# Performance work log

Hardware: AMD Instinct MI355X
Metric: run time of the kernel (lower is better)

Reference implementation:

```python
import jax, jax.numpy as jnp
import numpy as np

B, T, D = 2, 2048, 1024
N, H = 16, 64  # num_heads, head_dim
LOG2E = 1.442695041
NEG_INF = -1.0e9


def setup_inputs() -> dict:
    key = jax.random.key(0)
    ks = jax.random.split(key, 6)
    return {
        "input_tensor": jax.random.normal(ks[0], (B, T, D), dtype=jnp.float32),
        "attention_mask": jax.random.randint(ks[1], (B, 1, T, T), 0, 2, dtype=jnp.int32),
        "wq": jax.random.normal(ks[2], (D, N, H), dtype=jnp.float32),
        "bq": jnp.zeros((N, H), dtype=jnp.float32),
        "wk": jax.random.normal(ks[3], (D, N, H), dtype=jnp.float32),
        "bk": jnp.zeros((N, H), dtype=jnp.float32),
        "wv": jax.random.normal(ks[4], (D, N, H), dtype=jnp.float32),
        "bv": jnp.zeros((N, H), dtype=jnp.float32),
        "wo": jax.random.normal(ks[5], (D, N, H), dtype=jnp.float32),
        "bo": jnp.zeros((D,), dtype=jnp.float32),
        "per_dim_scale": jnp.zeros((H,), dtype=jnp.float32),
    }


def reference(input_tensor, attention_mask, wq, bq, wk, bk, wv, bv, wo, bo, per_dim_scale):
    # QKV projections: [B,T,D] x [D,N,H] -> [B,T,N,H]
    q = jnp.einsum('btd,dnh->btnh', input_tensor, wq) + bq
    k = jnp.einsum('btd,dnh->btnh', input_tensor, wk) + bk
    v = jnp.einsum('btd,dnh->btnh', input_tensor, wv) + bv
    # per-dim query scaling: (log2(e)/sqrt(H)) * softplus(per_dim_scale)
    scale = (LOG2E / jnp.sqrt(jnp.asarray(H, q.dtype))) * jax.nn.softplus(per_dim_scale)
    q = q * scale
    # scores: [B,N,T,S]
    scores = jnp.einsum('btnh,bsnh->bnts', q, k)
    scores = jnp.where(attention_mask == 0, jnp.asarray(NEG_INF, scores.dtype), scores)
    weights = jax.nn.softmax(scores, axis=-1)
    # AV: [B,N,T,S] x [B,S,N,H] -> [B,T,N,H]
    attn_out = jnp.einsum('bnts,bsnh->btnh', weights, v)
    # output projection: [B,T,N,H] x [D,N,H] -> [B,T,D]
    return jnp.einsum('btnh,dnh->btd', attn_out, wo) + bo
```

## Files before the change

### kernel.cpp

```cpp
#include <hip/hip_runtime.h>
#include <math.h>

typedef __bf16 bf16;
typedef __attribute__((ext_vector_type(8))) __bf16 bf16x8;
typedef __attribute__((ext_vector_type(4))) __bf16 bf16x4;
typedef __attribute__((ext_vector_type(4))) float f32x4;

#define BB 2
#define TT 2048
#define DD 1024
#define NHD 16
#define HD 64
#define MM (BB*TT)
#define LOG2E_F 1.442695041f
#define NEGINF_F (-1.0e9f)

__device__ __forceinline__ void gld16(const bf16* g, bf16* l)
{
    __builtin_amdgcn_global_load_lds(
        (const __attribute__((address_space(1))) unsigned int*)g,
        (__attribute__((address_space(3))) unsigned int*)l, 16, 0, 0);
}

__global__ __launch_bounds__(256)
void prep_all(const float* __restrict__ X, const int* __restrict__ m,
              const float* __restrict__ wq, const float* __restrict__ wk,
              const float* __restrict__ wv, const float* __restrict__ wo,
              bf16* __restrict__ Xh, bf16* __restrict__ Xl,
              bf16* __restrict__ qkh, bf16* __restrict__ qkl,
              bf16* __restrict__ vh, bf16* __restrict__ ob,
              bf16* __restrict__ madd)
{
    __shared__ float tile[32][33];
    const int bid = blockIdx.x;
    const int t   = threadIdx.x;

    if (bid < 4096) {
        int i = bid * 256 + t;
        float4 v = ((const float4*)X)[i];
        float f[4] = {v.x, v.y, v.z, v.w};
        bf16x4 h, l;
        #pragma unroll
        for (int j = 0; j < 4; ++j) {
            bf16 hh = (bf16)f[j];
            h[j] = hh;
            l[j] = (bf16)(f[j] - (float)hh);
        }
        *(bf16x4*)(Xh + (size_t)i * 4) = h;
        *(bf16x4*)(Xl + (size_t)i * 4) = l;
        return;
    }
    if (bid < 8192) {
        const int idx = bid - 4096;
        const int z   = idx >> 10;
        const int bx  = (idx & 31) << 5;
        const int by  = ((idx >> 5) & 31) << 5;
        const int r   = t >> 3;
        const int c4  = (t & 7) << 2;
        if (z == 3) {
            float4 v = *(const float4*)(wo + (size_t)(by + r) * 1024 + bx + c4);
            bf16x4 o = { (bf16)v.x, (bf16)v.y, (bf16)v.z, (bf16)v.w };
            *(bf16x4*)(ob + (size_t)(by + r) * 1024 + bx + c4) = o;
            return;
        }
        const float* src = (z == 0) ? wq : ((z == 1) ? wk : wv);
        bf16* oh = (z == 0) ? qkh : ((z == 1) ? qkh + 1048576 : vh);
        bf16* ol = (z == 0) ? qkl : ((z == 1) ? qkl + 1048576 : nullptr);
        float4 v = *(const float4*)(src + (size_t)(by + r) * 1024 + bx + c4);
        tile[r][c4+0] = v.x; tile[r][c4+1] = v.y;
        tile[r][c4+2] = v.z; tile[r][c4+3] = v.w;
        __syncthreads();
        bf16x4 hv, lv;
        #pragma unroll
        for (int j = 0; j < 4; ++j) {
            float f = tile[c4 + j][r];
            bf16 h = (bf16)f;
            hv[j] = h;
            lv[j] = (bf16)(f - (float)h);
        }
        *(bf16x4*)(oh + (size_t)(bx + r) * 1024 + by + c4) = hv;
        if (ol)
            *(bf16x4*)(ol + (size_t)(bx + r) * 1024 + by + c4) = lv;
        return;
    }
    {
        int i = (bid - 8192) * 256 + t;
        const int4* mp = (const int4*)m + (size_t)i * 2;
        int4 a  = mp[0];
        int4 b4 = mp[1];
        bf16x8 o;
        o[0] = (bf16)(a.x  ? 0.f : NEGINF_F);
        o[1] = (bf16)(a.y  ? 0.f : NEGINF_F);
        o[2] = (bf16)(a.z  ? 0.f : NEGINF_F);
        o[3] = (bf16)(a.w  ? 0.f : NEGINF_F);
        o[4] = (bf16)(b4.x ? 0.f : NEGINF_F);
        o[5] = (bf16)(b4.y ? 0.f : NEGINF_F);
        o[6] = (bf16)(b4.z ? 0.f : NEGINF_F);
        o[7] = (bf16)(b4.w ? 0.f : NEGINF_F);
        *(bf16x8*)(madd + (size_t)i * 8) = o;
    }
}

__global__ __launch_bounds__(256)
void gemm_proj(const bf16* __restrict__ Xh, const bf16* __restrict__ Xl,
               const bf16* __restrict__ Wh, const bf16* __restrict__ Wl,
               const bf16* __restrict__ Wvh,
               const float* __restrict__ bq, const float* __restrict__ bk,
               const float* __restrict__ bv, const float* __restrict__ pds,
               bf16* __restrict__ oQh, bf16* __restrict__ oQl,
               bf16* __restrict__ oKh, bf16* __restrict__ oKl,
               bf16* __restrict__ oVt)
{
    __shared__ bf16 S[4][128 * 32];

    const int bid  = blockIdx.x;
    const int t    = threadIdx.x;
    const int lane = t & 63;
    const int w    = t >> 6;
    const int quad = lane >> 4, l15 = lane & 15;
    const int wm   = (w >> 1) << 6;
    const int wn   = (w & 1)  << 6;

    const int jr0 = ((w * 2 + 0) << 4) + (lane >> 2);
    const int jr1 = ((w * 2 + 1) << 4) + (lane >> 2);
    const int kch = (lane & 3) << 3;
    const int off0 = (w * 2 + 0) * 512;
    const int off1 = (w * 2 + 1) * 512;

    if (bid < 512) {
        const int m0 = (bid >> 4) << 7;
        const int n0 = (bid & 15) << 7;
        bf16* Ah = S[0]; bf16* Al = S[1]; bf16* Bh = S[2]; bf16* Bl = S[3];

        const bf16* pAh0 = Xh + (size_t)(m0 + jr0) * DD + kch;
        const bf16* pAh1 = Xh + (size_t)(m0 + jr1) * DD + kch;
        const bf16* pAl0 = Xl + (size_t)(m0 + jr0) * DD + kch;
        const bf16* pAl1 = Xl + (size_t)(m0 + jr1) * DD + kch;
        const bf16* pBh0 = Wh + (size_t)(n0 + jr0) * DD + kch;
        const bf16* pBh1 = Wh + (size_t)(n0 + jr1) * DD + kch;
        const bf16* pBl0 = Wl + (size_t)(n0 + jr0) * DD + kch;
        const bf16* pBl1 = Wl + (size_t)(n0 + jr1) * DD + kch;

        f32x4 acc[4][4] = {};

        for (int k0 = 0; k0 < DD; k0 += 32) {
            __syncthreads();
            gld16(pAh0 + k0, Ah + off0);  gld16(pAh1 + k0, Ah + off1);
            gld16(pAl0 + k0, Al + off0);  gld16(pAl1 + k0, Al + off1);
            gld16(pBh0 + k0, Bh + off0);  gld16(pBh1 + k0, Bh + off1);
            gld16(pBl0 + k0, Bl + off0);  gld16(pBl1 + k0, Bl + off1);
            __syncthreads();

            bf16x8 ah[4], bh[4];
            #pragma unroll
            for (int mt = 0; mt < 4; ++mt)
                ah[mt] = *(const bf16x8*)(Ah + (wm + (mt << 4) + l15) * 32 + (quad << 3));
            #pragma unroll
            for (int nt = 0; nt < 4; ++nt)
                bh[nt] = *(const bf16x8*)(Bh + (wn + (nt << 4) + l15) * 32 + (quad << 3));
            #pragma unroll
            for (int mt = 0; mt < 4; ++mt)
                #pragma unroll
                for (int nt = 0; nt < 4; ++nt)
                    acc[mt][nt] = __builtin_amdgcn_mfma_f32_16x16x32_bf16(
                        ah[mt], bh[nt], acc[mt][nt], 0, 0, 0);

            bf16x8 bl[4];
            #pragma unroll
            for (int nt = 0; nt < 4; ++nt)
                bl[nt] = *(const bf16x8*)(Bl + (wn + (nt << 4) + l15) * 32 + (quad << 3));
            #pragma unroll
            for (int mt = 0; mt < 4; ++mt)
                #pragma unroll
                for (int nt = 0; nt < 4; ++nt)
                    acc[mt][nt] = __builtin_amdgcn_mfma_f32_16x16x32_bf16(
                        ah[mt], bl[nt], acc[mt][nt], 0, 0, 0);

            bf16x8 al[4];
            #pragma unroll
            for (int mt = 0; mt < 4; ++mt)
                al[mt] = *(const bf16x8*)(Al + (wm + (mt << 4) + l15) * 32 + (quad << 3));
            #pragma unroll
            for (int mt = 0; mt < 4; ++mt)
                #pragma unroll
                for (int nt = 0; nt < 4; ++nt)
                    acc[mt][nt] = __builtin_amdgcn_mfma_f32_16x16x32_bf16(
                        al[mt], bh[nt], acc[mt][nt], 0, 0, 0);
        }

        #pragma unroll
        for (int nt = 0; nt < 4; ++nt) {
            const int col = n0 + wn + (nt << 4) + l15;
            const int isQ = (col < 1024);
            const int nh  = col & 1023;
            const int n   = nh >> 6, h = nh & 63;
            const float bcol = isQ ? bq[nh] : bk[nh];
            float s = 1.f;
            if (isQ) {
                float x  = pds[h];
                float sp = fmaxf(x, 0.f) + log1pf(expf(-fabsf(x)));
                s = (LOG2E_F * LOG2E_F / 8.0f) * sp;
            }
            bf16* dH = isQ ? oQh : oKh;
            bf16* dL = isQ ? oQl : oKl;
            #pragma unroll
            for (int mt = 0; mt < 4; ++mt) {
                #pragma unroll
                for (int reg = 0; reg < 4; ++reg) {
                    const int row = m0 + wm + (mt << 4) + (quad << 2) + reg;
                    const int bi  = row >> 11;
                    const int tt  = row & (TT - 1);
                    float val = (acc[mt][nt][reg] + bcol) * s;
                    const size_t idx = (((size_t)bi * NHD + n) * TT + tt) * HD + h;
                    bf16 hi = (bf16)val;
                    dH[idx] = hi;
                    dL[idx] = (bf16)(val - (float)hi);
                }
            }
        }
    } else {
        const int idx = bid - 512;
        const int m0  = (idx >> 5) << 7;
        const int n0  = (idx & 31) << 7;
        bf16* As = S[0]; bf16* Bs = S[2];

        const bf16* Ap0 = Wvh + (size_t)(m0 + jr0) * DD + kch;
        const bf16* Ap1 = Wvh + (size_t)(m0 + jr1) * DD + kch;
        const bf16* Bp0 = Xh  + (size_t)(n0 + jr0) * DD + kch;
        const bf16* Bp1 = Xh  + (size_t)(n0 + jr1) * DD + kch;

        f32x4 acc[4][4] = {};

        for (int k0 = 0; k0 < DD; k0 += 32) {
            __syncthreads();
            gld16(Ap0 + k0, As + off0);
            gld16(Ap1 + k0, As + off1);
            gld16(Bp0 + k0, Bs + off0);
            gld16(Bp1 + k0, Bs + off1);
            __syncthreads();
            bf16x8 af[4], bfm[4];
            #pragma unroll
            for (int mt = 0; mt < 4; ++mt)
                af[mt] = *(const bf16x8*)(As + (wm + (mt << 4) + l15) * 32 + (quad << 3));
            #pragma unroll
            for (int nt = 0; nt < 4; ++nt)
                bfm[nt] = *(const bf16x8*)(Bs + (wn + (nt << 4) + l15) * 32 + (quad << 3));
            #pragma unroll
            for (int mt = 0; mt < 4; ++mt)
                #pragma unroll
                for (int nt = 0; nt < 4; ++nt)
                    acc[mt][nt] = __builtin_amdgcn_mfma_f32_16x16x32_bf16(
                        af[mt], bfm[nt], acc[mt][nt], 0, 0, 0);
        }

        #pragma unroll
        for (int nt = 0; nt < 4; ++nt) {
            const int col = n0 + wn + (nt << 4) + l15;
            const int bi  = col >> 11;
            const int tt  = col & (TT - 1);
            #pragma unroll
            for (int mt = 0; mt < 4; ++mt) {
                #pragma unroll
                for (int reg = 0; reg < 4; ++reg) {
                    const int row = m0 + wm + (mt << 4) + (quad << 2) + reg;
                    float val = acc[mt][nt][reg] + bv[row];
                    oVt[((size_t)bi * 1024 + row) * TT + tt] = (bf16)val;
                }
            }
        }
    }
}

__global__ __launch_bounds__(256)
void gemm_out(const bf16* __restrict__ A, const bf16* __restrict__ Bt,
              const float* __restrict__ bias, float* __restrict__ oF)
{
    __shared__ bf16 As[128 * 32];
    __shared__ bf16 Bs[64 * 32];

    const int t    = threadIdx.x;
    const int lane = t & 63;
    const int w    = t >> 6;
    const int quad = lane >> 4, l15 = lane & 15;
    const int m0   = blockIdx.y << 7;
    const int n0   = blockIdx.x << 6;
    const int wm   = (w >> 1) << 6;
    const int wn   = (w & 1)  << 5;

    const int jr0 = ((w * 2 + 0) << 4) + (lane >> 2);
    const int jr1 = ((w * 2 + 1) << 4) + (lane >> 2);
    const int jrB = (w << 4) + (lane >> 2);
    const int kch = (lane & 3) << 3;

    bf16* lA0 = As + (w * 2 + 0) * 512;
    bf16* lA1 = As + (w * 2 + 1) * 512;
    bf16* lB  = Bs + w * 512;

    const bf16* Ap0 = A  + (size_t)(m0 + jr0) * DD + kch;
    const bf16* Ap1 = A  + (size_t)(m0 + jr1) * DD + kch;
    const bf16* Bp  = Bt + (size_t)(n0 + jrB) * DD + kch;

    f32x4 acc[4][2] = {};

    for (int k0 = 0; k0 < DD; k0 += 32) {
        __syncthreads();
        gld16(Ap0 + k0, lA0);
        gld16(Ap1 + k0, lA1);
        gld16(Bp + k0, lB);
        __syncthreads();
        bf16x8 af[4], bfm[2];
        #pragma unroll
        for (int mt = 0; mt < 4; ++mt)
            af[mt] = *(const bf16x8*)(As + (wm + (mt << 4) + l15) * 32 + (quad << 3));
        #pragma unroll
        for (int nt = 0; nt < 2; ++nt)
            bfm[nt] = *(const bf16x8*)(Bs + (wn + (nt << 4) + l15) * 32 + (quad << 3));
        #pragma unroll
        for (int mt = 0; mt < 4; ++mt)
            #pragma unroll
            for (int nt = 0; nt < 2; ++nt)
                acc[mt][nt] = __builtin_amdgcn_mfma_f32_16x16x32_bf16(
                    af[mt], bfm[nt], acc[mt][nt], 0, 0, 0);
    }

    #pragma unroll
    for (int nt = 0; nt < 2; ++nt) {
        const int col = n0 + wn + (nt << 4) + l15;
        const float bcol = bias[col];
        #pragma unroll
        for (int mt = 0; mt < 4; ++mt) {
            #pragma unroll
            for (int reg = 0; reg < 4; ++reg) {
                const int row = m0 + wm + (mt << 4) + (quad << 2) + reg;
                oF[(size_t)row * DD + col] = acc[mt][nt][reg] + bcol;
            }
        }
    }
}

__global__ __launch_bounds__(512)
void attn_mfma(const bf16* __restrict__ Qh, const bf16* __restrict__ Ql,
               const bf16* __restrict__ Kh, const bf16* __restrict__ Kl,
               const bf16* __restrict__ Vt,
               const bf16* __restrict__ Madd,
               bf16* __restrict__ AO)
{
    __shared__ bf16 Ksh[64 * 64];
    __shared__ bf16 Ksl[64 * 64];
    __shared__ bf16 Vts[64 * 64];
    __shared__ bf16 MT [128 * 64];
    __shared__ bf16 PS [8][16 * 64];

    const int t    = threadIdx.x;
    const int lane = t & 63;
    const int w    = t >> 6;
    const int quad = lane >> 4, l15 = lane & 15;
    const int bn   = blockIdx.y;
    const int b    = bn >> 4, n = bn & 15;
    const int q0   = blockIdx.x << 7;

    const bf16* Qbh = Qh + (size_t)bn * TT * HD;
    const bf16* Qbl = Ql + (size_t)bn * TT * HD;
    const bf16* Kbh = Kh + (size_t)bn * TT * HD;
    const bf16* Kbl = Kl + (size_t)bn * TT * HD;
    const bf16* Vtb = Vt + (size_t)bn * HD * TT;
    const bf16* Mb  = Madd + (size_t)b * TT * TT;

    const int qrow = q0 + (w << 4) + l15;
    bf16x8 qfh[2], qfl[2];
    qfh[0] = *(const bf16x8*)(Qbh + (size_t)qrow * HD + (quad << 3));
    qfh[1] = *(const bf16x8*)(Qbh + (size_t)qrow * HD + 32 + (quad << 3));
    qfl[0] = *(const bf16x8*)(Qbl + (size_t)qrow * HD + (quad << 3));
    qfl[1] = *(const bf16x8*)(Qbl + (size_t)qrow * HD + 32 + (quad << 3));

    f32x4 O[4];
    #pragma unroll
    for (int i = 0; i < 4; ++i) O[i] = (f32x4){0.f,0.f,0.f,0.f};
    float m_i = -INFINITY;
    float l_i = 0.f;

    const int rS = t >> 3;
    const int cG = (t & 7) << 3;
    const int cL = (((t & 7) ^ (rS & 7)) << 3);
    const int sw8 = (l15 & 7) << 3;
    const int qtr = (w << 4) + l15;

    for (int kb = 0; kb < TT; kb += 64) {
        bf16x8 khv = *(const bf16x8*)(Kbh + (size_t)(kb + rS) * HD + cG);
        bf16x8 klv = *(const bf16x8*)(Kbl + (size_t)(kb + rS) * HD + cG);
        bf16x8 vv  = *(const bf16x8*)(Vtb + (size_t)rS * TT + kb + cG);
        const bf16* mrow = Mb + (size_t)(q0 + rS) * TT + kb;
        bf16x8 m0v = *(const bf16x8*)(mrow + cG);
        bf16x8 m1v = *(const bf16x8*)(mrow + (size_t)64 * TT + cG);

        __syncthreads();
        *(bf16x8*)&Ksh[rS * 64 + cL] = khv;
        *(bf16x8*)&Ksl[rS * 64 + cL] = klv;
        *(bf16x8*)&Vts[rS * 64 + cL] = vv;
        *(bf16x8*)&MT [rS * 64 + cL]        = m0v;
        *(bf16x8*)&MT [(64 + rS) * 64 + cL] = m1v;
        __syncthreads();

        f32x4 s_acc[4];
        #pragma unroll
        for (int nt = 0; nt < 4; ++nt) {
            const int moff = ((((nt << 1) + (quad >> 1)) ^ (l15 & 7)) << 3)
                             + ((quad & 1) << 2);
            ushort4 mu = *(const ushort4*)&MT[qtr * 64 + moff];
            s_acc[nt][0] = __uint_as_float((unsigned)mu.x << 16);
            s_acc[nt][1] = __uint_as_float((unsigned)mu.y << 16);
            s_acc[nt][2] = __uint_as_float((unsigned)mu.z << 16);
            s_acc[nt][3] = __uint_as_float((unsigned)mu.w << 16);
        }

        __builtin_amdgcn_s_setprio(1);
        #pragma unroll
        for (int k2 = 0; k2 < 2; ++k2) {
            #pragma unroll
            for (int nt = 0; nt < 4; ++nt) {
                const int ro = ((nt << 4) + l15) * 64;
                const int co = ((k2 << 5) + (quad << 3)) ^ sw8;
                bf16x8 bkh = *(const bf16x8*)&Ksh[ro + co];
                bf16x8 bkl = *(const bf16x8*)&Ksl[ro + co];
                s_acc[nt] = __builtin_amdgcn_mfma_f32_16x16x32_bf16(bkh, qfh[k2], s_acc[nt], 0, 0, 0);
                s_acc[nt] = __builtin_amdgcn_mfma_f32_16x16x32_bf16(bkl, qfh[k2], s_acc[nt], 0, 0, 0);
                s_acc[nt] = __builtin_amdgcn_mfma_f32_16x16x32_bf16(bkh, qfl[k2], s_acc[nt], 0, 0, 0);
            }
        }
        __builtin_amdgcn_s_setprio(0);

        float t0 = fmaxf(fmaxf(s_acc[0][0], s_acc[0][1]), s_acc[0][2]);
        float t1 = fmaxf(fmaxf(s_acc[0][3], s_acc[1][0]), s_acc[1][1]);
        float t2 = fmaxf(fmaxf(s_acc[1][2], s_acc[1][3]), s_acc[2][0]);
        float t3 = fmaxf(fmaxf(s_acc[2][1], s_acc[2][2]), s_acc[2][3]);
        float t4 = fmaxf(fmaxf(s_acc[3][0], s_acc[3][1]), s_acc[3][2]);
        float mx = fmaxf(fmaxf(fmaxf(t0, t1), t2),
                         fmaxf(fmaxf(t3, t4), s_acc[3][3]));
        mx = fmaxf(mx, __shfl_xor(mx, 16));
        mx = fmaxf(mx, __shfl_xor(mx, 32));

        if (!__all(mx <= m_i + 8.0f)) {
            const float mnew  = fmaxf(m_i, mx);
            const float alpha = exp2f(m_i - mnew);
            l_i *= alpha;
            #pragma unroll
            for (int nt = 0; nt < 4; ++nt) {
                O[nt][0] *= alpha; O[nt][1] *= alpha;
                O[nt][2] *= alpha; O[nt][3] *= alpha;
            }
            m_i = mnew;
        }

        float p[16];
        #pragma unroll
        for (int nt = 0; nt < 4; ++nt)
            #pragma unroll
            for (int reg = 0; reg < 4; ++reg)
                p[nt * 4 + reg] = exp2f(s_acc[nt][reg] - m_i);
        float s0 = (p[0] + p[1]) + (p[2] + p[3]);
        float s1 = (p[4] + p[5]) + (p[6] + p[7]);
        float s2 = (p[8] + p[9]) + (p[10] + p[11]);
        float s3 = (p[12] + p[13]) + (p[14] + p[15]);
        float sum = (s0 + s1) + (s2 + s3);
        sum += __shfl_xor(sum, 16);
        sum += __shfl_xor(sum, 32);
        l_i += sum;

        #pragma unroll
        for (int nt = 0; nt < 4; ++nt) {
            bf16x4 pv = { (bf16)p[nt * 4 + 0], (bf16)p[nt * 4 + 1],
                          (bf16)p[nt * 4 + 2], (bf16)p[nt * 4 + 3] };
            *(bf16x4*)&PS[w][l15 * 64 + (((nt << 4) + (quad << 2)) ^ sw8)] = pv;
        }

        __builtin_amdgcn_s_setprio(1);
        #pragma unroll
        for (int s2i = 0; s2i < 2; ++s2i) {
            bf16x8 ap = *(const bf16x8*)&PS[w][l15 * 64 + (((s2i << 5) + (quad << 3)) ^ sw8)];
            #pragma unroll
            for (int nt = 0; nt < 4; ++nt) {
                bf16x8 bv = *(const bf16x8*)&Vts[((nt << 4) + l15) * 64
                                                 + (((s2i << 5) + (quad << 3)) ^ sw8)];
                O[nt] = __builtin_amdgcn_mfma_f32_16x16x32_bf16(bv, ap, O[nt], 0, 0, 0);
            }
        }
        __builtin_amdgcn_s_setprio(0);
    }

    {
        const float inv = 1.0f / l_i;
        const size_t base = ((size_t)b * TT + qrow) * (NHD * HD) + (size_t)n * HD;
        #pragma unroll
        for (int nt = 0; nt < 4; ++nt) {
            bf16x4 o = { (bf16)(O[nt][0] * inv), (bf16)(O[nt][1] * inv),
                         (bf16)(O[nt][2] * inv), (bf16)(O[nt][3] * inv) };
            *(bf16x4*)(AO + base + (nt << 4) + (quad << 2)) = o;
        }
    }
}

extern "C" void kernel_launch(void* const* d_in, const int* in_sizes, int n_in,
                              void* d_out, int out_size, void* d_ws, size_t ws_size,
                              hipStream_t stream)
{
    const float* X   = (const float*)d_in[0];
    const int*   msk = (const int*)d_in[1];
    const float* wq  = (const float*)d_in[2];
    const float* bq  = (const float*)d_in[3];
    const float* wk  = (const float*)d_in[4];
    const float* bk  = (const float*)d_in[5];
    const float* wv  = (const float*)d_in[6];
    const float* bv  = (const float*)d_in[7];
    const float* wo  = (const float*)d_in[8];
    const float* bo  = (const float*)d_in[9];
    const float* pds = (const float*)d_in[10];
    float* out = (float*)d_out;

    bf16* ws   = (bf16*)d_ws;
    bf16* Xh   = ws;
    bf16* Xl   = ws + 4194304;
    bf16* WQKh = ws + 8388608;
    bf16* WQKl = ws + 10485760;
    bf16* Wvh  = ws + 12582912;
    bf16* Wob  = ws + 13631488;
    bf16* Qhb  = ws + 14680064;
    bf16* Qlb  = ws + 18874368;
    bf16* Khb  = ws + 23068672;
    bf16* Klb  = ws + 27262976;
    bf16* Vtb  = ws + 32505856;
    bf16* AOb  = Xh;
    bf16* madd = (bf16*)d_out;

    dim3 blk(256);

    prep_all<<<12288, blk, 0, stream>>>(X, msk, wq, wk, wv, wo,
                                        Xh, Xl, WQKh, WQKl, Wvh, Wob, madd);

    gemm_proj<<<768, blk, 0, stream>>>(
        Xh, Xl, WQKh, WQKl, Wvh, bq, bk, bv, pds,
        Qhb, Qlb, Khb, Klb, Vtb);

    dim3 ga(TT / 128, BB * NHD);
    attn_mfma<<<ga, dim3(512), 0, stream>>>(
        Qhb, Qlb, Khb, Klb, Vtb, madd, AOb);

    gemm_out<<<dim3(16, 32), blk, 0, stream>>>(AOb, Wob, bo, out);
}
```

Baseline: 310.5 us.

## Compute softmax row sum via MFMA, load mask directly, swizzle projection block order

The attention kernel drops the shared-memory mask tile and has each lane read its own mask values straight from global memory into registers, which removes LDS writes and reads per key block. The softmax denominator is now accumulated by an extra MFMA of a ones vector against the bf16 probabilities, replacing the scalar sum and cross-lane shuffles. As a side effect the denominator now uses bf16-rounded probabilities, which matches the values used in the AV product. The projection GEMM also remaps block indices so that consecutively launched blocks cover different row tiles, intended to change cache reuse. The direct mask loads are 8-byte strided reads and may coalesce less well than the previous tiled loads.

```diff
diff --git a/kernel.cpp b/kernel.cpp
--- a/kernel.cpp
+++ b/kernel.cpp
@@ -113,7 +113,13 @@
 {
     __shared__ bf16 S[4][128 * 32];
 
-    const int bid  = blockIdx.x;
+    int bid = blockIdx.x;
+    if (bid < 512) bid = ((bid & 7) << 6) + (bid >> 3);
+    else {
+        int idx = bid - 512;
+        bid = 512 + (((idx & 7) << 5) + (idx >> 3));
+    }
+
     const int t    = threadIdx.x;
     const int lane = t & 63;
     const int w    = t >> 6;
@@ -348,7 +354,6 @@
     __shared__ bf16 Ksh[64 * 64];
     __shared__ bf16 Ksl[64 * 64];
     __shared__ bf16 Vts[64 * 64];
-    __shared__ bf16 MT [128 * 64];
     __shared__ bf16 PS [8][16 * 64];
 
     const int t    = threadIdx.x;
@@ -376,42 +381,52 @@
     f32x4 O[4];
     #pragma unroll
     for (int i = 0; i < 4; ++i) O[i] = (f32x4){0.f,0.f,0.f,0.f};
+    f32x4 Ol = (f32x4){0.f,0.f,0.f,0.f};
     float m_i = -INFINITY;
-    float l_i = 0.f;
+
+    const bf16 onev = (bf16)1.0f;
+    const bf16x8 ones = { onev, onev, onev, onev, onev, onev, onev, onev };
 
     const int rS = t >> 3;
     const int cG = (t & 7) << 3;
     const int cL = (((t & 7) ^ (rS & 7)) << 3);
     const int sw8 = (l15 & 7) << 3;
-    const int qtr = (w << 4) + l15;
+
+    const bf16* mrow0 = Mb + (size_t)qrow * TT + (quad << 2);
 
     for (int kb = 0; kb < TT; kb += 64) {
         bf16x8 khv = *(const bf16x8*)(Kbh + (size_t)(kb + rS) * HD + cG);
         bf16x8 klv = *(const bf16x8*)(Kbl + (size_t)(kb + rS) * HD + cG);
         bf16x8 vv  = *(const bf16x8*)(Vtb + (size_t)rS * TT + kb + cG);
-        const bf16* mrow = Mb + (size_t)(q0 + rS) * TT + kb;
-        bf16x8 m0v = *(const bf16x8*)(mrow + cG);
-        bf16x8 m1v = *(const bf16x8*)(mrow + (size_t)64 * TT + cG);
+        const bf16* mr = mrow0 + kb;
+        ushort4 mu0 = *(const ushort4*)(mr);
+        ushort4 mu1 = *(const ushort4*)(mr + 16);
+        ushort4 mu2 = *(const ushort4*)(mr + 32);
+        ushort4 mu3 = *(const ushort4*)(mr + 48);
 
         __syncthreads();
         *(bf16x8*)&Ksh[rS * 64 + cL] = khv;
         *(bf16x8*)&Ksl[rS * 64 + cL] = klv;
         *(bf16x8*)&Vts[rS * 64 + cL] = vv;
-        *(bf16x8*)&MT [rS * 64 + cL]        = m0v;
-        *(bf16x8*)&MT [(64 + rS) * 64 + cL] = m1v;
         __syncthreads();
 
         f32x4 s_acc[4];
-        #pragma unroll
-        for (int nt = 0; nt < 4; ++nt) {
-            const int moff = ((((nt << 1) + (quad >> 1)) ^ (l15 & 7)) << 3)
-                             + ((quad & 1) << 2);
-            ushort4 mu = *(const ushort4*)&MT[qtr * 64 + moff];
-            s_acc[nt][0] = __uint_as_float((unsigned)mu.x << 16);
-            s_acc[nt][1] = __uint_as_float((unsigned)mu.y << 16);
-            s_acc[nt][2] = __uint_as_float((unsigned)mu.z << 16);
-            s_acc[nt][3] = __uint_as_float((unsigned)mu.w << 16);
-        }
+        s_acc[0][0] = __uint_as_float((unsigned)mu0.x << 16);
+        s_acc[0][1] = __uint_as_float((unsigned)mu0.y << 16);
+        s_acc[0][2] = __uint_as_float((unsigned)mu0.z << 16);
+        s_acc[0][3] = __uint_as_float((unsigned)mu0.w << 16);
+        s_acc[1][0] = __uint_as_float((unsigned)mu1.x << 16);
+        s_acc[1][1] = __uint_as_float((unsigned)mu1.y << 16);
+        s_acc[1][2] = __uint_as_float((unsigned)mu1.z << 16);
+        s_acc[1][3] = __uint_as_float((unsigned)mu1.w << 16);
+        s_acc[2][0] = __uint_as_float((unsigned)mu2.x << 16);
+        s_acc[2][1] = __uint_as_float((unsigned)mu2.y << 16);
+        s_acc[2][2] = __uint_as_float((unsigned)mu2.z << 16);
+        s_acc[2][3] = __uint_as_float((unsigned)mu2.w << 16);
+        s_acc[3][0] = __uint_as_float((unsigned)mu3.x << 16);
+        s_acc[3][1] = __uint_as_float((unsigned)mu3.y << 16);
+        s_acc[3][2] = __uint_as_float((unsigned)mu3.z << 16);
+        s_acc[3][3] = __uint_as_float((unsigned)mu3.w << 16);
 
         __builtin_amdgcn_s_setprio(1);
         #pragma unroll
@@ -442,12 +457,12 @@
         if (!__all(mx <= m_i + 8.0f)) {
             const float mnew  = fmaxf(m_i, mx);
             const float alpha = exp2f(m_i - mnew);
-            l_i *= alpha;
             #pragma unroll
             for (int nt = 0; nt < 4; ++nt) {
                 O[nt][0] *= alpha; O[nt][1] *= alpha;
                 O[nt][2] *= alpha; O[nt][3] *= alpha;
             }
+            Ol[0] *= alpha; Ol[1] *= alpha; Ol[2] *= alpha; Ol[3] *= alpha;
             m_i = mnew;
         }
 
@@ -457,14 +472,6 @@
             #pragma unroll
             for (int reg = 0; reg < 4; ++reg)
                 p[nt * 4 + reg] = exp2f(s_acc[nt][reg] - m_i);
-        float s0 = (p[0] + p[1]) + (p[2] + p[3]);
-        float s1 = (p[4] + p[5]) + (p[6] + p[7]);
-        float s2 = (p[8] + p[9]) + (p[10] + p[11]);
-        float s3 = (p[12] + p[13]) + (p[14] + p[15]);
-        float sum = (s0 + s1) + (s2 + s3);
-        sum += __shfl_xor(sum, 16);
-        sum += __shfl_xor(sum, 32);
-        l_i += sum;
 
         #pragma unroll
         for (int nt = 0; nt < 4; ++nt) {
@@ -477,6 +484,7 @@
         #pragma unroll
         for (int s2i = 0; s2i < 2; ++s2i) {
             bf16x8 ap = *(const bf16x8*)&PS[w][l15 * 64 + (((s2i << 5) + (quad << 3)) ^ sw8)];
+            Ol = __builtin_amdgcn_mfma_f32_16x16x32_bf16(ones, ap, Ol, 0, 0, 0);
             #pragma unroll
             for (int nt = 0; nt < 4; ++nt) {
                 bf16x8 bv = *(const bf16x8*)&Vts[((nt << 4) + l15) * 64
@@ -488,7 +496,7 @@
     }
 
     {
-        const float inv = 1.0f / l_i;
+        const float inv = 1.0f / Ol[0];
         const size_t base = ((size_t)b * TT + qrow) * (NHD * HD) + (size_t)n * HD;
         #pragma unroll
         for (int nt = 0; nt < 4; ++nt) {
```

After: 305.7 us. No clear change (-1.5%).
